# Kernel optimization log

Measured on AMD Instinct MI355X. Metric: run time of the kernel, lower is better.

The kernel has to match this reference:

```python
import jax, jax.numpy as jnp
import numpy as np

B, S, D, E, K, F = 2, 1024, 1024, 8, 2, 2048


def setup_inputs() -> dict:
    key = jax.random.key(0)
    k0, k1, k2, k3 = jax.random.split(key, 4)
    x = jax.random.normal(k0, (B, S, D), dtype=jnp.float32)
    gate_w = (jax.random.normal(k1, (E, D), dtype=jnp.float32) * 0.02)  # nn.init.normal_(std=0.02)
    # nn.Linear default init ~ U(-1/sqrt(fan_in), 1/sqrt(fan_in)); use same scale
    w1 = jax.random.uniform(k2, (E, F, D), dtype=jnp.float32, minval=-1.0, maxval=1.0) / np.float32(np.sqrt(D))
    w2 = jax.random.uniform(k3, (E, D, F), dtype=jnp.float32, minval=-1.0, maxval=1.0) / np.float32(np.sqrt(F))
    norm_w = jnp.ones((D,), dtype=jnp.float32)
    scale = jnp.full((1,), -4.0, dtype=jnp.float32)
    return {"x": x, "gate_w": gate_w, "w1": w1, "w2": w2, "norm_w": norm_w, "scale": scale}


def reference(x, gate_w, w1, w2, norm_w, scale):
    b, s, d = x.shape
    e = gate_w.shape[0]
    t = b * s
    eps = jnp.finfo(x.dtype).eps  # torch RMSNorm eps=None -> dtype eps
    # RMSNorm
    xn = x * jax.lax.rsqrt(jnp.mean(x * x, axis=-1, keepdims=True) + eps) * norm_w
    xf = xn.reshape(t, d)
    # router
    logits = xf @ gate_w.T                       # [T, E]
    prob = jax.nn.softmax(logits, axis=-1)
    topk_w, topk_e = jax.lax.top_k(prob, K)      # [T, K]
    topk_w = topk_w / jnp.clip(jnp.sum(topk_w, axis=-1, keepdims=True), 1e-6)
    # dense combine weights [T, E]: sum of slot weights routed to each expert
    combine = jnp.sum(jax.nn.one_hot(topk_e, e, dtype=xf.dtype) * topk_w[..., None], axis=1)
    # all-expert FFN, weighted combine (same math as the gather/index_add loop)
    h = jax.nn.silu(jnp.einsum('td,efd->tef', xf, w1))   # [T, E, F]
    out = jnp.einsum('tef,edf,te->td', h, w2, combine)    # [T, D]
    # load-balance aux loss (Switch eq.4), f_e from top-1 slot, detached
    f_e = jnp.mean(jax.nn.one_hot(topk_e[:, 0], e, dtype=prob.dtype), axis=0)
    lb_loss = e * jnp.sum(jax.lax.stop_gradient(f_e) * jnp.mean(prob, axis=0))
    sc = jax.nn.sigmoid(scale)[0]
    return (x + sc * out.reshape(b, s, d), lb_loss)
```

## Files before the change

kernel.cpp:

```cpp
#include <hip/hip_runtime.h>
#include <stdint.h>

#define T_TOK 2048
#define DD 1024
#define EE 8
#define FF 2048
#define NSLOT 4096
#define SLOTPAD 4224

typedef __attribute__((ext_vector_type(8))) __bf16 bf16x8;
typedef __attribute__((ext_vector_type(4))) float floatx4;

__device__ __forceinline__ unsigned short f2bf(float f){
  union { float f; unsigned u; } v; v.f = f;
  unsigned r = v.u + 0x7fffu + ((v.u >> 16) & 1u);
  return (unsigned short)(r >> 16);
}

__global__ __launch_bounds__(256) void k_cvt_bf16(const float* __restrict__ in,
    unsigned short* __restrict__ out, int n4)
{
  int i = blockIdx.x * 256 + threadIdx.x;
  const int stride = gridDim.x * 256;
  for (; i < n4; i += stride){
    const float4 v = ((const float4*)in)[i];
    ushort4 o; o.x = f2bf(v.x); o.y = f2bf(v.y); o.z = f2bf(v.z); o.w = f2bf(v.w);
    ((ushort4*)out)[i] = o;
  }
}

__global__ __launch_bounds__(256) void k_rms_router(
    const float* __restrict__ x, const float* __restrict__ gw,
    const float* __restrict__ nw,
    unsigned short* __restrict__ xn,
    int* __restrict__ topk_id, float* __restrict__ topk_w,
    float* __restrict__ probbuf)
{
  const int t = blockIdx.x, tid = threadIdx.x;
  const float4 xv = ((const float4*)(x + (size_t)t * DD))[tid];
  float ss = xv.x*xv.x + xv.y*xv.y + xv.z*xv.z + xv.w*xv.w;
  #pragma unroll
  for (int o = 32; o > 0; o >>= 1) ss += __shfl_down(ss, o);
  __shared__ float s_ss[4];
  __shared__ float s_p[4][8];
  if ((tid & 63) == 0) s_ss[tid >> 6] = ss;
  __syncthreads();
  const float tot = s_ss[0] + s_ss[1] + s_ss[2] + s_ss[3];
  const float inv = rsqrtf(tot * (1.0f / DD) + 1.1920929e-7f);
  const float4 nv = ((const float4*)nw)[tid];
  float4 xnv;
  xnv.x = xv.x*inv*nv.x; xnv.y = xv.y*inv*nv.y;
  xnv.z = xv.z*inv*nv.z; xnv.w = xv.w*inv*nv.w;
  ushort4 bv; bv.x = f2bf(xnv.x); bv.y = f2bf(xnv.y); bv.z = f2bf(xnv.z); bv.w = f2bf(xnv.w);
  ((ushort4*)(xn + (size_t)t * DD))[tid] = bv;
  float p[8];
  #pragma unroll
  for (int e = 0; e < 8; e++){
    const float4 g = ((const float4*)(gw + e * DD))[tid];
    p[e] = xnv.x*g.x + xnv.y*g.y + xnv.z*g.z + xnv.w*g.w;
  }
  #pragma unroll
  for (int e = 0; e < 8; e++){
    #pragma unroll
    for (int o = 32; o > 0; o >>= 1) p[e] += __shfl_down(p[e], o);
  }
  if ((tid & 63) == 0){
    #pragma unroll
    for (int e = 0; e < 8; e++) s_p[tid >> 6][e] = p[e];
  }
  __syncthreads();
  if (tid == 0){
    float lg[8], pr[8];
    #pragma unroll
    for (int e = 0; e < 8; e++) lg[e] = s_p[0][e] + s_p[1][e] + s_p[2][e] + s_p[3][e];
    float mx = lg[0];
    for (int e = 1; e < 8; e++) mx = fmaxf(mx, lg[e]);
    float sum = 0.f;
    for (int e = 0; e < 8; e++){ pr[e] = __expf(lg[e] - mx); sum += pr[e]; }
    const float is = 1.f / sum;
    for (int e = 0; e < 8; e++) pr[e] *= is;
    #pragma unroll
    for (int e = 0; e < 8; e++) probbuf[t * 8 + e] = pr[e];
    int e1 = 0;
    for (int e = 1; e < 8; e++) if (pr[e] > pr[e1]) e1 = e;
    int e2 = (e1 == 0) ? 1 : 0;
    for (int e = 0; e < 8; e++) if (e != e1 && e != e2 && pr[e] > pr[e2]) e2 = e;
    const float wsum = fmaxf(pr[e1] + pr[e2], 1e-6f);
    topk_id[2*t] = e1; topk_id[2*t+1] = e2;
    topk_w[2*t] = pr[e1] / wsum; topk_w[2*t+1] = pr[e2] / wsum;
  }
}

__global__ __launch_bounds__(256) void k_stats(
    const int* __restrict__ topk_id, const float* __restrict__ topk_w,
    const float* __restrict__ probbuf,
    int* __restrict__ counts, int* __restrict__ bases,
    int* __restrict__ slots_of, int* __restrict__ tok_of,
    float* __restrict__ slot_w,
    float* __restrict__ lb_out)
{
  const int tid = threadIdx.x;
  __shared__ int s_scan[256][8];
  __shared__ int s_base[8];

  int ids[16];
  int lc[8] = {}, lc1[8] = {};
  float lsp[8] = {};
  #pragma unroll
  for (int j = 0; j < 8; j++){
    const int t = tid * 8 + j;
    const int e1 = topk_id[2*t], e2 = topk_id[2*t+1];
    ids[2*j] = e1; ids[2*j+1] = e2;
    lc[e1]++; lc[e2]++; lc1[e1]++;
    const float4 p0 = ((const float4*)(probbuf + t * 8))[0];
    const float4 p1 = ((const float4*)(probbuf + t * 8))[1];
    lsp[0] += p0.x; lsp[1] += p0.y; lsp[2] += p0.z; lsp[3] += p0.w;
    lsp[4] += p1.x; lsp[5] += p1.y; lsp[6] += p1.z; lsp[7] += p1.w;
  }
  #pragma unroll
  for (int e = 0; e < 8; e++) s_scan[tid][e] = lc[e];
  __syncthreads();
  for (int off = 1; off < 256; off <<= 1){
    int v[8];
    if (tid >= off){
      #pragma unroll
      for (int e = 0; e < 8; e++) v[e] = s_scan[tid - off][e];
    }
    __syncthreads();
    if (tid >= off){
      #pragma unroll
      for (int e = 0; e < 8; e++) s_scan[tid][e] += v[e];
    }
    __syncthreads();
  }
  int   rc1[8]; float rsp[8];
  #pragma unroll
  for (int e = 0; e < 8; e++){ rc1[e] = lc1[e]; rsp[e] = lsp[e]; }
  #pragma unroll
  for (int e = 0; e < 8; e++){
    #pragma unroll
    for (int o = 32; o > 0; o >>= 1){
      rc1[e] += __shfl_down(rc1[e], o);
      rsp[e] += __shfl_down(rsp[e], o);
    }
  }
  __shared__ int   s_c1[4][8];
  __shared__ float s_sp[4][8];
  if ((tid & 63) == 0){
    const int w = tid >> 6;
    #pragma unroll
    for (int e = 0; e < 8; e++){ s_c1[w][e] = rc1[e]; s_sp[w][e] = rsp[e]; }
  }
  __syncthreads();
  if (tid == 0){
    int b = 0; float lb = 0.f;
    for (int e = 0; e < 8; e++){
      const int tot = s_scan[255][e];
      counts[e] = tot; bases[e] = b; s_base[e] = b; b += tot;
      const int   c1 = s_c1[0][e] + s_c1[1][e] + s_c1[2][e] + s_c1[3][e];
      const float sp = s_sp[0][e] + s_sp[1][e] + s_sp[2][e] + s_sp[3][e];
      lb += (float)c1 * sp;
    }
    lb_out[0] = 8.f * lb * (1.f / ((float)T_TOK * (float)T_TOK));
  }
  __syncthreads();
  int rank[8];
  #pragma unroll
  for (int e = 0; e < 8; e++) rank[e] = s_scan[tid][e] - lc[e];
  #pragma unroll
  for (int j = 0; j < 8; j++){
    const int t = tid * 8 + j;
    #pragma unroll
    for (int k = 0; k < 2; k++){
      const int e = ids[2*j + k];
      const int slot = s_base[e] + rank[e]++;
      slots_of[2*t + k] = slot;
      tok_of[slot] = t;
      slot_w[slot] = topk_w[2*t + k];
    }
  }
}

template<int KDIM, int NDIM, int MODE>
__global__ __launch_bounds__(256) void k_gemm(
    const unsigned short* __restrict__ Ag,
    const unsigned short* __restrict__ Bw,
    const int* __restrict__ counts, const int* __restrict__ bases,
    const int* __restrict__ tok_of,
    const float* __restrict__ slot_w,
    void* __restrict__ Cout)
{
  constexpr int NT = NDIM / 128;
  const int bpe = 16 * NT;
  const int e   = blockIdx.x / bpe;
  const int rem = blockIdx.x - e * bpe;
  const int mt  = rem / NT;
  const int nt  = rem - mt * NT;
  const int M = counts[e];
  if (mt * 128 >= M) return;
  const int sbase = bases[e];

  __shared__ __align__(16) unsigned short As[128 * 32];
  __shared__ __align__(16) unsigned short Bs[128 * 32];

  const int tid = threadIdx.x;
  const int l = tid & 63;
  const int w = tid >> 6;
  const int wm = (w >> 1) * 64, wn = (w & 1) * 64;
  const int lrow = l & 15, lk = (l >> 4) * 8;

  const unsigned short* arow[2];
  #pragma unroll
  for (int i = 0; i < 2; i++){
    const int c = tid + i * 256;
    const int row = c >> 2;
    if (MODE == 0){
      const int slot = min(sbase + mt * 128 + row, NSLOT - 1);
      arow[i] = Ag + (size_t)tok_of[slot] * KDIM;
    } else {
      arow[i] = Ag + (size_t)(sbase + mt * 128 + row) * KDIM;
    }
  }
  const unsigned short* B0 = Bw + (size_t)e * NDIM * KDIM + (size_t)(nt * 128) * KDIM;

  floatx4 acc[4][4] = {};

  for (int k0 = 0; k0 < KDIM; k0 += 32){
    #pragma unroll
    for (int i = 0; i < 2; i++){
      const int c = tid + i * 256;
      const int row = c >> 2, kc = c & 3;
      const unsigned short* ga = arow[i] + k0 + kc * 8;
      const unsigned short* gb = B0 + (size_t)row * KDIM + k0 + kc * 8;
      __builtin_amdgcn_global_load_lds(
          (__attribute__((address_space(1))) unsigned int*)ga,
          (__attribute__((address_space(3))) unsigned int*)(As + c * 8), 16, 0, 0);
      __builtin_amdgcn_global_load_lds(
          (__attribute__((address_space(1))) unsigned int*)gb,
          (__attribute__((address_space(3))) unsigned int*)(Bs + c * 8), 16, 0, 0);
    }
    __syncthreads();
    bf16x8 af[4], bfv[4];
    #pragma unroll
    for (int mi = 0; mi < 4; mi++)
      af[mi] = *(const bf16x8*)(As + (wm + mi * 16 + lrow) * 32 + lk);
    #pragma unroll
    for (int ni = 0; ni < 4; ni++)
      bfv[ni] = *(const bf16x8*)(Bs + (wn + ni * 16 + lrow) * 32 + lk);
    #pragma unroll
    for (int mi = 0; mi < 4; mi++)
      #pragma unroll
      for (int ni = 0; ni < 4; ni++)
        acc[mi][ni] = __builtin_amdgcn_mfma_f32_16x16x32_bf16(af[mi], bfv[ni], acc[mi][ni], 0, 0, 0);
    __syncthreads();
  }

  const int rb = (l >> 4) * 4;
  #pragma unroll
  for (int mi = 0; mi < 4; mi++){
    #pragma unroll
    for (int r = 0; r < 4; r++){
      const int row = mt * 128 + wm + mi * 16 + rb + r;
      if (row < M){
        #pragma unroll
        for (int ni = 0; ni < 4; ni++){
          const int col = nt * 128 + wn + ni * 16 + (l & 15);
          const float v = acc[mi][ni][r];
          if (MODE == 0){
            const float s = v / (1.f + __expf(-v));
            ((unsigned short*)Cout)[(size_t)(sbase + row) * NDIM + col] = f2bf(s);
          } else {
            const float wgt = slot_w[sbase + row];
            ((float*)Cout)[(size_t)(sbase + row) * NDIM + col] = v * wgt;
          }
        }
      }
    }
  }
}

__global__ __launch_bounds__(256) void k_combine(
    const float* __restrict__ x, const float* __restrict__ Og,
    const int* __restrict__ slots_of, const float* __restrict__ scale,
    float* __restrict__ out)
{
  const int i = blockIdx.x * 256 + threadIdx.x;
  const int t = i >> 8;
  const int j = i & 255;
  const int s0 = slots_of[2*t], s1 = slots_of[2*t+1];
  const float4 a = ((const float4*)(Og + (size_t)s0 * DD))[j];
  const float4 b = ((const float4*)(Og + (size_t)s1 * DD))[j];
  const float4 xv = ((const float4*)x)[i];
  const float sc = 1.f / (1.f + __expf(-scale[0]));
  float4 o;
  o.x = xv.x + sc * (a.x + b.x);
  o.y = xv.y + sc * (a.y + b.y);
  o.z = xv.z + sc * (a.z + b.z);
  o.w = xv.w + sc * (a.w + b.w);
  ((float4*)out)[i] = o;
}

extern "C" void kernel_launch(void* const* d_in, const int* in_sizes, int n_in,
                              void* d_out, int out_size, void* d_ws, size_t ws_size,
                              hipStream_t stream)
{
  const float* x     = (const float*)d_in[0];
  const float* gw    = (const float*)d_in[1];
  const float* w1    = (const float*)d_in[2];
  const float* w2    = (const float*)d_in[3];
  const float* nw    = (const float*)d_in[4];
  const float* scale = (const float*)d_in[5];
  float* out = (float*)d_out;

  char* ws = (char*)d_ws;
  int*   counts  = (int*)(ws + 0);
  int*   bases   = (int*)(ws + 64);
  int*   topk_id = (int*)(ws + 1024);
  float* topk_w  = (float*)(ws + 20480);
  int*   slots_of= (int*)(ws + 40960);
  float* slot_w  = (float*)(ws + 61440);
  int*   tok_of  = (int*)(ws + 81920);
  float* probbuf = (float*)(ws + 102400);
  unsigned short* xn  = (unsigned short*)(ws + 262144);
  unsigned short* Hg  = xn + (size_t)T_TOK * DD;
  float*          Og  = (float*)(Hg + (size_t)SLOTPAD * FF);
  unsigned short* w1b = (unsigned short*)(Og + (size_t)SLOTPAD * DD);
  unsigned short* w2b = w1b + (size_t)EE * FF * DD;

  k_cvt_bf16<<<8192, 256, 0, stream>>>(w1, w1b, EE*FF*DD/4);
  k_cvt_bf16<<<8192, 256, 0, stream>>>(w2, w2b, EE*DD*FF/4);
  k_rms_router<<<T_TOK, 256, 0, stream>>>(x, gw, nw, xn, topk_id, topk_w, probbuf);
  k_stats<<<1, 256, 0, stream>>>(topk_id, topk_w, probbuf, counts, bases,
                                 slots_of, tok_of, slot_w, out + (size_t)T_TOK * DD);
  k_gemm<1024, 2048, 0><<<EE * 16 * (FF/128), 256, 0, stream>>>(xn, w1b, counts, bases, tok_of, nullptr, Hg);
  k_gemm<2048, 1024, 1><<<EE * 16 * (DD/128), 256, 0, stream>>>(Hg, w2b, counts, bases, nullptr, slot_w, Og);
  k_combine<<<T_TOK * DD / 4 / 256, 256, 0, stream>>>(x, Og, slots_of, scale, out);
}
```

Baseline: 283.7 us.

## Fuse weight conversion into router kernel, swizzle GEMM LDS, interleave expert blocks

Merges the two fp32-to-bf16 weight conversion launches and the RMSNorm/router kernel into one launch, using extra blocks for conversion. This removes launch gaps and lets the conversion overlap the per-token router work. The GEMM now XOR-style rotates the k-chunk placement in LDS to reduce bank conflicts on fragment reads. It also reorders the block index so consecutive blocks belong to different experts, spreading early-exit blocks across the grid.

```diff
diff --git a/kernel.cpp b/kernel.cpp
--- a/kernel.cpp
+++ b/kernel.cpp
@@ -7,6 +7,7 @@
 #define FF 2048
 #define NSLOT 4096
 #define SLOTPAD 4224
+#define CVT_BLOCKS 6144
 
 typedef __attribute__((ext_vector_type(8))) __bf16 bf16x8;
 typedef __attribute__((ext_vector_type(4))) float floatx4;
@@ -17,26 +18,29 @@
   return (unsigned short)(r >> 16);
 }
 
-__global__ __launch_bounds__(256) void k_cvt_bf16(const float* __restrict__ in,
-    unsigned short* __restrict__ out, int n4)
-{
-  int i = blockIdx.x * 256 + threadIdx.x;
-  const int stride = gridDim.x * 256;
-  for (; i < n4; i += stride){
-    const float4 v = ((const float4*)in)[i];
-    ushort4 o; o.x = f2bf(v.x); o.y = f2bf(v.y); o.z = f2bf(v.z); o.w = f2bf(v.w);
-    ((ushort4*)out)[i] = o;
-  }
-}
-
-__global__ __launch_bounds__(256) void k_rms_router(
+__global__ __launch_bounds__(256) void k_front(
     const float* __restrict__ x, const float* __restrict__ gw,
     const float* __restrict__ nw,
+    const float* __restrict__ w1, const float* __restrict__ w2,
     unsigned short* __restrict__ xn,
     int* __restrict__ topk_id, float* __restrict__ topk_w,
-    float* __restrict__ probbuf)
-{
-  const int t = blockIdx.x, tid = threadIdx.x;
+    float* __restrict__ probbuf,
+    unsigned short* __restrict__ w1b, unsigned short* __restrict__ w2b)
+{
+  const int tid = threadIdx.x;
+  if (blockIdx.x >= T_TOK){
+    const int n4 = EE * FF * DD / 4;
+    int i = (blockIdx.x - T_TOK) * 256 + tid;
+    const int stride = CVT_BLOCKS * 256;
+    for (; i < 2 * n4; i += stride){
+      const int j = (i < n4) ? i : i - n4;
+      const float4 v = (i < n4) ? ((const float4*)w1)[j] : ((const float4*)w2)[j];
+      ushort4 o; o.x = f2bf(v.x); o.y = f2bf(v.y); o.z = f2bf(v.z); o.w = f2bf(v.w);
+      if (i < n4) ((ushort4*)w1b)[j] = o; else ((ushort4*)w2b)[j] = o;
+    }
+    return;
+  }
+  const int t = blockIdx.x;
   const float4 xv = ((const float4*)(x + (size_t)t * DD))[tid];
   float ss = xv.x*xv.x + xv.y*xv.y + xv.z*xv.z + xv.w*xv.w;
   #pragma unroll
@@ -191,11 +195,10 @@
     void* __restrict__ Cout)
 {
   constexpr int NT = NDIM / 128;
-  const int bpe = 16 * NT;
-  const int e   = blockIdx.x / bpe;
-  const int rem = blockIdx.x - e * bpe;
-  const int mt  = rem / NT;
-  const int nt  = rem - mt * NT;
+  const int e  = blockIdx.x & 7;
+  const int g  = blockIdx.x >> 3;
+  const int mt = g / NT;
+  const int nt = g - mt * NT;
   const int M = counts[e];
   if (mt * 128 >= M) return;
   const int sbase = bases[e];
@@ -207,13 +210,15 @@
   const int l = tid & 63;
   const int w = tid >> 6;
   const int wm = (w >> 1) * 64, wn = (w & 1) * 64;
-  const int lrow = l & 15, lk = (l >> 4) * 8;
+  const int lrow = l & 15, lq = l >> 4;
 
   const unsigned short* arow[2];
+  int kcs[2];
   #pragma unroll
   for (int i = 0; i < 2; i++){
     const int c = tid + i * 256;
-    const int row = c >> 2;
+    const int row = c >> 2, q = c & 3;
+    kcs[i] = ((q - (row >> 1)) & 3) * 8;
     if (MODE == 0){
       const int slot = min(sbase + mt * 128 + row, NSLOT - 1);
       arow[i] = Ag + (size_t)tok_of[slot] * KDIM;
@@ -229,9 +234,9 @@
     #pragma unroll
     for (int i = 0; i < 2; i++){
       const int c = tid + i * 256;
-      const int row = c >> 2, kc = c & 3;
-      const unsigned short* ga = arow[i] + k0 + kc * 8;
-      const unsigned short* gb = B0 + (size_t)row * KDIM + k0 + kc * 8;
+      const int row = c >> 2;
+      const unsigned short* ga = arow[i] + k0 + kcs[i];
+      const unsigned short* gb = B0 + (size_t)row * KDIM + k0 + kcs[i];
       __builtin_amdgcn_global_load_lds(
           (__attribute__((address_space(1))) unsigned int*)ga,
           (__attribute__((address_space(3))) unsigned int*)(As + c * 8), 16, 0, 0);
@@ -242,11 +247,17 @@
     __syncthreads();
     bf16x8 af[4], bfv[4];
     #pragma unroll
-    for (int mi = 0; mi < 4; mi++)
-      af[mi] = *(const bf16x8*)(As + (wm + mi * 16 + lrow) * 32 + lk);
-    #pragma unroll
-    for (int ni = 0; ni < 4; ni++)
-      bfv[ni] = *(const bf16x8*)(Bs + (wn + ni * 16 + lrow) * 32 + lk);
+    for (int mi = 0; mi < 4; mi++){
+      const int row = wm + mi * 16 + lrow;
+      const int p = (lq + (row >> 1)) & 3;
+      af[mi] = *(const bf16x8*)(As + row * 32 + p * 8);
+    }
+    #pragma unroll
+    for (int ni = 0; ni < 4; ni++){
+      const int row = wn + ni * 16 + lrow;
+      const int p = (lq + (row >> 1)) & 3;
+      bfv[ni] = *(const bf16x8*)(Bs + row * 32 + p * 8);
+    }
     #pragma unroll
     for (int mi = 0; mi < 4; mi++)
       #pragma unroll
@@ -255,7 +266,7 @@
     __syncthreads();
   }
 
-  const int rb = (l >> 4) * 4;
+  const int rb = lq * 4;
   #pragma unroll
   for (int mi = 0; mi < 4; mi++){
     #pragma unroll
@@ -327,9 +338,8 @@
   unsigned short* w1b = (unsigned short*)(Og + (size_t)SLOTPAD * DD);
   unsigned short* w2b = w1b + (size_t)EE * FF * DD;
 
-  k_cvt_bf16<<<8192, 256, 0, stream>>>(w1, w1b, EE*FF*DD/4);
-  k_cvt_bf16<<<8192, 256, 0, stream>>>(w2, w2b, EE*DD*FF/4);
-  k_rms_router<<<T_TOK, 256, 0, stream>>>(x, gw, nw, xn, topk_id, topk_w, probbuf);
+  k_front<<<T_TOK + CVT_BLOCKS, 256, 0, stream>>>(x, gw, nw, w1, w2, xn,
+                                                  topk_id, topk_w, probbuf, w1b, w2b);
   k_stats<<<1, 256, 0, stream>>>(topk_id, topk_w, probbuf, counts, bases,
                                  slots_of, tok_of, slot_w, out + (size_t)T_TOK * DD);
   k_gemm<1024, 2048, 0><<<EE * 16 * (FF/128), 256, 0, stream>>>(xn, w1b, counts, bases, tok_of, nullptr, Hg);
```

Measured after the change: 274.5 us. -3.3%, faster.
